# Optimization experiments

Measured on AMD Instinct MI355X. Metric: run time of the kernel, lower is better.

## Reference

```python
import jax, jax.numpy as jnp
import numpy as np

N_NODES = 100000
N_EDGES = 1600000
N_GRAPHS = 256
DIMS = [128, 128, 128, 128]  # gcn_layers_dim -> 3 GCNConv layers


def setup_inputs() -> dict:
    key = jax.random.key(0)
    ks = jax.random.split(key, 12)
    inp = {
        "x": jax.random.normal(ks[0], (N_NODES, DIMS[0]), jnp.float32),
        "edge_index": jax.random.randint(ks[1], (2, N_EDGES), 0, N_NODES),
        "edge_weight": jax.random.uniform(ks[2], (N_EDGES,), jnp.float32),
        "batch": jnp.sort(jax.random.randint(ks[3], (N_NODES,), 0, N_GRAPHS)),
    }
    for i in range(3):
        fan_in = DIMS[i]
        scale = 1.0 / np.sqrt(fan_in)
        inp[f"W{i+1}"] = jax.random.uniform(ks[4 + 2 * i], (DIMS[i], DIMS[i + 1]),
                                             jnp.float32, -scale, scale)
        inp[f"b{i+1}"] = jax.random.uniform(ks[5 + 2 * i], (DIMS[i + 1],),
                                             jnp.float32, -scale, scale)
    return inp


def reference(x, edge_index, edge_weight, batch, W1, b1, W2, b2, W3, b3):
    n = x.shape[0]
    # PyG GCNConv: add self-loops with weight 1, symmetric normalization.
    loop = jnp.arange(n)
    row = jnp.concatenate([edge_index[0], loop])  # source nodes
    col = jnp.concatenate([edge_index[1], loop])  # target nodes (aggregation index)
    w = jnp.concatenate([edge_weight, jnp.ones((n,), x.dtype)])
    deg = jax.ops.segment_sum(w, col, num_segments=n)
    dinv = jnp.where(deg > 0, jax.lax.rsqrt(deg), jnp.zeros_like(deg))
    norm = dinv[row] * w * dinv[col]  # [E+N]

    # global_mean_pool setup
    counts = jax.ops.segment_sum(jnp.ones((n,), x.dtype), batch,
                                 num_segments=N_GRAPHS)
    counts = jnp.maximum(counts, 1.0)[:, None]

    def gcn_conv(h, W, b):
        hl = h @ W                      # linear projection first (PyG order)
        msg = hl[row] * norm[:, None]   # gather + edge scaling
        out = jax.ops.segment_sum(msg, col, num_segments=n)  # scatter-add
        return out + b

    embeddings = []
    h = x
    for W, b in ((W1, b1), (W2, b2), (W3, b3)):
        h = gcn_conv(h, W, b)
        h = jax.nn.relu(h)              # relu_layers_index = [0,1,2]
        emb = jax.ops.segment_sum(h, batch, num_segments=N_GRAPHS) / counts
        embeddings.append(emb)          # gep = global_mean_pool
    return tuple(embeddings)
```

## Files before the change

kernel.cpp:

```cpp
#include <hip/hip_runtime.h>


typedef short short8 __attribute__((ext_vector_type(8)));
typedef float f32x4  __attribute__((ext_vector_type(4)));

__device__ inline unsigned pack_bf16x2(float a, float b) {
    unsigned ua = __float_as_uint(a);
    ua = (ua + 0x7FFFu + ((ua >> 16) & 1u)) >> 16;
    unsigned ub = __float_as_uint(b);
    ub = (ub + 0x7FFFu + ((ub >> 16) & 1u)) >> 16;
    return ua | (ub << 16);
}
__device__ inline ushort bf16_1(float a) {
    unsigned ua = __float_as_uint(a);
    return (ushort)((ua + 0x7FFFu + ((ua >> 16) & 1u)) >> 16);
}
__device__ inline float bf_lo(unsigned u) { return __uint_as_float(u << 16); }
__device__ inline float bf_hi(unsigned u) { return __uint_as_float(u & 0xFFFF0000u); }

__global__ void k_zero(int* __restrict__ cnt, int N) {
    int i = blockIdx.x * blockDim.x + threadIdx.x;
    if (i < N) cnt[i] = 0;
}

__global__ void k_phase1(const int* __restrict__ ei, int* __restrict__ cnt,
                         int* __restrict__ epos, int E) {
    int e = blockIdx.x * blockDim.x + threadIdx.x;
    if (e >= E) return;
    int c = ei[E + e];
    epos[e] = atomicAdd(&cnt[c], 1);
}

__global__ __launch_bounds__(1024) void k_scan1(const int* __restrict__ cnt,
                                                int* __restrict__ pre,
                                                int* __restrict__ bsum, int n) {
    __shared__ int wsum[16];
    int t = threadIdx.x, lane = t & 63, w = t >> 6;
    int i = blockIdx.x * 1024 + t;
    int v = (i < n) ? cnt[i] : 0;
    int x = v;
#pragma unroll
    for (int off = 1; off < 64; off <<= 1) {
        int y = __shfl_up(x, off, 64);
        if (lane >= off) x += y;
    }
    if (lane == 63) wsum[w] = x;
    __syncthreads();
    int woff = 0, tot = 0;
#pragma unroll
    for (int q = 0; q < 16; q++) { int s = wsum[q]; if (q < w) woff += s; tot += s; }
    if (i < n) pre[i] = woff + x - v;
    if (t == 0) bsum[blockIdx.x] = tot;
}

__global__ __launch_bounds__(128) void k_scan2(int* __restrict__ bsum, int nb,
                                               int* __restrict__ ptrv, int n) {
    __shared__ int ws[2];
    int t = threadIdx.x, lane = t & 63, w = t >> 6;
    int v = (t < nb) ? bsum[t] : 0;
    int x = v;
#pragma unroll
    for (int off = 1; off < 64; off <<= 1) {
        int y = __shfl_up(x, off, 64);
        if (lane >= off) x += y;
    }
    if (lane == 63) ws[w] = x;
    __syncthreads();
    int woff = (w == 1) ? ws[0] : 0;
    int tot = ws[0] + ws[1];
    if (t < nb) bsum[t] = woff + x - v;
    if (t == 0) ptrv[n] = tot;
}

__global__ __launch_bounds__(1024) void k_scan3(const int* __restrict__ pre,
                                                const int* __restrict__ bsum,
                                                int* __restrict__ ptrv, int n) {
    int i = blockIdx.x * 1024 + threadIdx.x;
    if (i >= n) return;
    ptrv[i] = pre[i] + bsum[blockIdx.x];
}

__global__ void k_scatter(const int* __restrict__ ei, const float* __restrict__ ew,
                          const int* __restrict__ ptrv, const int* __restrict__ epos,
                          int2* __restrict__ csr, int E) {
    int e = blockIdx.x * blockDim.x + threadIdx.x;
    if (e >= E) return;
    int r = ei[e];
    int c = ei[E + e];
    int2 v; v.x = r; v.y = __float_as_int(ew[e]);
    csr[ptrv[c] + epos[e]] = v;
}

__global__ void k_degdinv(const int2* __restrict__ csr, const int* __restrict__ ptrv,
                          float* __restrict__ dinv, int N) {
    int i = blockIdx.x * blockDim.x + threadIdx.x;
    if (i >= N) return;
    float s = 1.0f;
    int e1 = ptrv[i + 1];
    for (int j = ptrv[i]; j < e1; j++) s += __int_as_float(csr[j].y);
    dinv[i] = (s > 0.f) ? rsqrtf(s) : 0.f;
}

__global__ void k_norm(int2* __restrict__ csr, const int* __restrict__ ptrv,
                       const float* __restrict__ dinv, int N) {
    int i = blockIdx.x * blockDim.x + threadIdx.x;
    if (i >= N) return;
    float dc = dinv[i];
    int e1 = ptrv[i + 1];
    for (int j = ptrv[i]; j < e1; j++) {
        int2 m = csr[j];
        m.y = __float_as_int(dinv[m.x] * __int_as_float(m.y) * dc);
        csr[j] = m;
    }
}

__global__ void k_bounds(const int* __restrict__ batch, int* __restrict__ gb,
                         int N, int G) {
    int t = blockIdx.x * blockDim.x + threadIdx.x;
    if (t > G) return;
    int lo = 0, hi = N;
    while (lo < hi) { int mid = (lo + hi) >> 1; if (batch[mid] < t) lo = mid + 1; else hi = mid; }
    gb[t] = lo;
}

__global__ void k_wprep(const float* __restrict__ W0, const float* __restrict__ W1,
                        const float* __restrict__ W2, ushort* __restrict__ WbT) {
    int l = blockIdx.y;
    const float* W = (l == 0) ? W0 : ((l == 1) ? W1 : W2);
    int id = blockIdx.x * 256 + threadIdx.x;
    int n = id & 127, k = id >> 7;
    WbT[l * 16384 + n * 128 + k] = bf16_1(W[k * 128 + n]);
}

template <bool F32IN>
__global__ __launch_bounds__(256) void k_gemm_mfma(const void* __restrict__ Hin,
                                                   const ushort* __restrict__ WbT,
                                                   unsigned* __restrict__ O, int M) {
    __shared__ unsigned sOut[4 * 32 * 64];
    int lane = threadIdx.x & 63;
    int wv = threadIdx.x >> 6;
    int quad = lane >> 4;
    int mrow = lane & 15;
    int m0 = blockIdx.x * 128 + wv * 32;
    int r0 = m0 + mrow;
    int r1 = r0 + 16;
    int r0c = r0 < M ? r0 : M - 1;
    int r1c = r1 < M ? r1 : M - 1;

    short8 a0[4], a1[4];
    if (F32IN) {
        const float* Hf = (const float*)Hin;
#pragma unroll
        for (int s = 0; s < 4; s++) {
            const float4* p0 = (const float4*)(Hf + (size_t)r0c * 128 + s * 32 + quad * 8);
            const float4* p1 = (const float4*)(Hf + (size_t)r1c * 128 + s * 32 + quad * 8);
            float4 f0 = p0[0], f1 = p0[1];
            float4 g0 = p1[0], g1 = p1[1];
            union { short8 s8; unsigned u[4]; } t0, t1;
            t0.u[0] = pack_bf16x2(f0.x, f0.y); t0.u[1] = pack_bf16x2(f0.z, f0.w);
            t0.u[2] = pack_bf16x2(f1.x, f1.y); t0.u[3] = pack_bf16x2(f1.z, f1.w);
            t1.u[0] = pack_bf16x2(g0.x, g0.y); t1.u[1] = pack_bf16x2(g0.z, g0.w);
            t1.u[2] = pack_bf16x2(g1.x, g1.y); t1.u[3] = pack_bf16x2(g1.z, g1.w);
            a0[s] = t0.s8; a1[s] = t1.s8;
        }
    } else {
        const unsigned* Hb = (const unsigned*)Hin;
#pragma unroll
        for (int s = 0; s < 4; s++) {
            a0[s] = *(const short8*)(Hb + (size_t)r0c * 64 + s * 16 + quad * 4);
            a1[s] = *(const short8*)(Hb + (size_t)r1c * 64 + s * 16 + quad * 4);
        }
    }
    f32x4 acc0[8], acc1[8];
#pragma unroll
    for (int t = 0; t < 8; t++) {
        acc0[t] = (f32x4){0.f, 0.f, 0.f, 0.f};
        acc1[t] = (f32x4){0.f, 0.f, 0.f, 0.f};
    }
#pragma unroll
    for (int s = 0; s < 4; s++) {
#pragma unroll
        for (int t = 0; t < 8; t++) {
            short8 b = *(const short8*)(WbT + (t * 16 + mrow) * 128 + s * 32 + quad * 8);
            acc0[t] = __builtin_amdgcn_mfma_f32_16x16x32_bf16(a0[s], b, acc0[t], 0, 0, 0);
            acc1[t] = __builtin_amdgcn_mfma_f32_16x16x32_bf16(a1[s], b, acc1[t], 0, 0, 0);
        }
    }
    ushort* so = (ushort*)(sOut + wv * 32 * 64);
#pragma unroll
    for (int t = 0; t < 8; t++) {
#pragma unroll
        for (int r = 0; r < 4; r++) {
            int lr = quad * 4 + r;
            int c = t * 16 + mrow;
            so[lr * 128 + c] = bf16_1(acc0[t][r]);
            so[(lr + 16) * 128 + c] = bf16_1(acc1[t][r]);
        }
    }
    __syncthreads();
    const unsigned* si = sOut + wv * 32 * 64;
#pragma unroll 8
    for (int r = 0; r < 32; r++) {
        int row = m0 + r;
        if (row < M) O[(size_t)row * 64 + lane] = si[r * 64 + lane];
    }
}

__global__ __launch_bounds__(256) void k_agg(const unsigned* __restrict__ HL,
                                             const int* __restrict__ ptr,
                                             const int2* __restrict__ csr,
                                             const float* __restrict__ dinv,
                                             const float* __restrict__ bias,
                                             unsigned* __restrict__ Hout, int M) {
    __shared__ int2 sM[4 * 64];
    int node = (int)((blockIdx.x * blockDim.x + threadIdx.x) >> 6);
    if (node >= M) return;
    int lane = threadIdx.x & 63;
    int half = lane >> 5;
    int q = lane & 31;
    int2* mbase = &sM[(threadIdx.x >> 6) * 64];
    int e0 = ptr[node], e1 = ptr[node + 1];
    int deg = e1 - e0;
    int nbv = deg < 64 ? deg : 64;
    if (lane < nbv) mbase[lane] = csr[e0 + lane];
    const uint2* HL2 = (const uint2*)HL;
    float di = dinv[node];
    float sn = (half == 0) ? di * di : 0.f;
    uint2 us = HL2[(size_t)node * 32 + q];
    float a0 = sn * bf_lo(us.x), a1 = sn * bf_hi(us.x);
    float a2 = sn * bf_lo(us.y), a3 = sn * bf_hi(us.y);
    int j = half;
    for (; j + 8 <= nbv; j += 8) {
        int2 m[4]; uint2 u[4];
#pragma unroll
        for (int t = 0; t < 4; t++) m[t] = mbase[j + 2 * t];
#pragma unroll
        for (int t = 0; t < 4; t++) u[t] = HL2[(size_t)m[t].x * 32 + q];
#pragma unroll
        for (int t = 0; t < 4; t++) {
            float nv = __int_as_float(m[t].y);
            a0 += nv * bf_lo(u[t].x); a1 += nv * bf_hi(u[t].x);
            a2 += nv * bf_lo(u[t].y); a3 += nv * bf_hi(u[t].y);
        }
    }
    for (; j < nbv; j += 2) {
        int2 m = mbase[j];
        uint2 u = HL2[(size_t)m.x * 32 + q];
        float nv = __int_as_float(m.y);
        a0 += nv * bf_lo(u.x); a1 += nv * bf_hi(u.x);
        a2 += nv * bf_lo(u.y); a3 += nv * bf_hi(u.y);
    }
    for (int e = e0 + 64 + half; e < e1; e += 2) {
        int2 m = csr[e];
        uint2 u = HL2[(size_t)m.x * 32 + q];
        float nv = __int_as_float(m.y);
        a0 += nv * bf_lo(u.x); a1 += nv * bf_hi(u.x);
        a2 += nv * bf_lo(u.y); a3 += nv * bf_hi(u.y);
    }
    a0 += __shfl_xor(a0, 32, 64);
    a1 += __shfl_xor(a1, 32, 64);
    a2 += __shfl_xor(a2, 32, 64);
    a3 += __shfl_xor(a3, 32, 64);
    float4 bv = ((const float4*)bias)[q];
    float r0 = fmaxf(a0 + bv.x, 0.f);
    float r1 = fmaxf(a1 + bv.y, 0.f);
    float r2 = fmaxf(a2 + bv.z, 0.f);
    float r3 = fmaxf(a3 + bv.w, 0.f);
    if (half == 0) {
        uint2 pv;
        pv.x = pack_bf16x2(r0, r1);
        pv.y = pack_bf16x2(r2, r3);
        ((uint2*)(Hout + (size_t)node * 64))[q] = pv;
    }
}

__global__ __launch_bounds__(256) void k_pool(const unsigned* __restrict__ HB,
                                              const int* __restrict__ gb,
                                              float* __restrict__ outp) {
    __shared__ float part[4][128];
    int g = blockIdx.x;
    int lane = threadIdx.x & 63, w = threadIdx.x >> 6;
    int s = gb[g], e = gb[g + 1];
    float ax = 0.f, ay = 0.f;
    for (int i = s + w; i < e; i += 4) {
        unsigned u = HB[(size_t)i * 64 + lane];
        ax += bf_lo(u); ay += bf_hi(u);
    }
    part[w][lane * 2] = ax;
    part[w][lane * 2 + 1] = ay;
    __syncthreads();
    if (threadIdx.x < 128) {
        float sum = part[0][threadIdx.x] + part[1][threadIdx.x]
                  + part[2][threadIdx.x] + part[3][threadIdx.x];
        float c = (float)(e - s);
        outp[g * 128 + threadIdx.x] = sum / fmaxf(c, 1.0f);
    }
}

extern "C" void kernel_launch(void* const* d_in, const int* in_sizes, int n_in,
                              void* d_out, int out_size, void* d_ws, size_t ws_size,
                              hipStream_t stream) {
    const float* x     = (const float*)d_in[0];
    const int*   ei    = (const int*)d_in[1];
    const float* ew    = (const float*)d_in[2];
    const int*   batch = (const int*)d_in[3];
    const float* Wt[3] = {(const float*)d_in[4], (const float*)d_in[6], (const float*)d_in[8]};
    const float* bt[3] = {(const float*)d_in[5], (const float*)d_in[7], (const float*)d_in[9]};
    float* out = (float*)d_out;

    const int D = 128;
    const int N = in_sizes[0] / D;
    const int E = in_sizes[2];
    const int G = out_size / (3 * D);

    char* p = (char*)d_ws;
    auto alloc = [&](size_t bytes) {
        void* r = (void*)p;
        p += (bytes + 255) & ~(size_t)255;
        return r;
    };
    int*      cnt    = (int*)alloc((size_t)N * 4);
    int*      ptr    = (int*)alloc((size_t)(N + 1) * 4);
    int*      pre    = (int*)alloc((size_t)N * 4);
    int*      bsum   = (int*)alloc((size_t)128 * 4);
    int*      gb     = (int*)alloc((size_t)(G + 1) * 4);
    float*    dinv   = (float*)alloc((size_t)N * 4);
    ushort*   WbT    = (ushort*)alloc((size_t)3 * 16384 * 2);
    int2*     csr    = (int2*)alloc((size_t)E * 8);
    unsigned* bufHL  = (unsigned*)alloc((size_t)N * 64 * 4);
    unsigned* bufH   = (unsigned*)alloc((size_t)N * 64 * 4);
    int*      epos   = (int*)bufH;

    int nb = (N + 1023) / 1024;

    k_zero<<<(N + 255) / 256, 256, 0, stream>>>(cnt, N);
    k_phase1<<<(E + 255) / 256, 256, 0, stream>>>(ei, cnt, epos, E);
    k_bounds<<<1, 512, 0, stream>>>(batch, gb, N, G);
    k_wprep<<<dim3(64, 3), 256, 0, stream>>>(Wt[0], Wt[1], Wt[2], WbT);
    k_scan1<<<nb, 1024, 0, stream>>>(cnt, pre, bsum, N);
    k_scan2<<<1, 128, 0, stream>>>(bsum, nb, ptr, N);
    k_scan3<<<nb, 1024, 0, stream>>>(pre, bsum, ptr, N);
    k_scatter<<<(E + 255) / 256, 256, 0, stream>>>(ei, ew, ptr, epos, csr, E);
    k_degdinv<<<(N + 255) / 256, 256, 0, stream>>>(csr, ptr, dinv, N);
    k_norm<<<(N + 255) / 256, 256, 0, stream>>>(csr, ptr, dinv, N);

    for (int l = 0; l < 3; l++) {
        if (l == 0)
            k_gemm_mfma<true><<<(N + 127) / 128, 256, 0, stream>>>(x, WbT, bufHL, N);
        else
            k_gemm_mfma<false><<<(N + 127) / 128, 256, 0, stream>>>(bufH, WbT + (size_t)l * 16384,
                                                                    bufHL, N);
        k_agg<<<(N + 3) / 4, 256, 0, stream>>>(bufHL, ptr, csr, dinv, bt[l], bufH, N);
        k_pool<<<G, 256, 0, stream>>>(bufH, gb, out + (size_t)l * G * D);
    }
}
```

Before: 600.7 us.

## Merge prep kernels, fold x bf16 cast into phase1, warp-parallel deg/norm

Combines the zero, bounds and weight-prep kernels into one launch. The fp32-to-bf16 cast of x moves into the edge-counting kernel so the first GEMM reads bf16 like the later layers. The degree and normalization kernels switch from one thread per node to 32 lanes per node with a shuffle reduction, which spreads the edge loop and coalesces CSR reads. This removes launches and serial per-thread loops, but it adds an extra bf16 copy of x in memory and a full write/read pass over it. It also drops the deg>0 guard, relying on the self-loop keeping s at least 1.

Measured after the change: 597.0 us. No clear change (-0.6%).

```diff
diff --git a/kernel.cpp b/kernel.cpp
--- a/kernel.cpp
+++ b/kernel.cpp
@@ -18,17 +18,43 @@
 __device__ inline float bf_lo(unsigned u) { return __uint_as_float(u << 16); }
 __device__ inline float bf_hi(unsigned u) { return __uint_as_float(u & 0xFFFF0000u); }
 
-__global__ void k_zero(int* __restrict__ cnt, int N) {
-    int i = blockIdx.x * blockDim.x + threadIdx.x;
-    if (i < N) cnt[i] = 0;
+__global__ void k_prep(int* __restrict__ cnt, int N,
+                       const int* __restrict__ batch, int* __restrict__ gb, int G,
+                       const float* __restrict__ W0, const float* __restrict__ W1,
+                       const float* __restrict__ W2, ushort* __restrict__ WbT) {
+    int id = blockIdx.x * blockDim.x + threadIdx.x;
+    if (id < N) cnt[id] = 0;
+    if (id <= G) {
+        int lo = 0, hi = N;
+        while (lo < hi) { int mid = (lo + hi) >> 1; if (batch[mid] < id) lo = mid + 1; else hi = mid; }
+        gb[id] = lo;
+    }
+    if (id < 3 * 16384) {
+        int l = id >> 14;
+        const float* W = (l == 0) ? W0 : ((l == 1) ? W1 : W2);
+        int id2 = id & 16383;
+        int n = id2 & 127, k = id2 >> 7;
+        WbT[l * 16384 + n * 128 + k] = bf16_1(W[k * 128 + n]);
+    }
 }
 
 __global__ void k_phase1(const int* __restrict__ ei, int* __restrict__ cnt,
-                         int* __restrict__ epos, int E) {
-    int e = blockIdx.x * blockDim.x + threadIdx.x;
-    if (e >= E) return;
-    int c = ei[E + e];
-    epos[e] = atomicAdd(&cnt[c], 1);
+                         int* __restrict__ epos, int E,
+                         const float4* __restrict__ x4, uint2* __restrict__ xb2,
+                         int nCast) {
+    int tid = blockIdx.x * blockDim.x + threadIdx.x;
+    if (tid < E) {
+        int c = ei[E + tid];
+        epos[tid] = atomicAdd(&cnt[c], 1);
+    }
+    int stride = gridDim.x * blockDim.x;
+    for (int i = tid; i < nCast; i += stride) {
+        float4 f = x4[i];
+        uint2 v;
+        v.x = pack_bf16x2(f.x, f.y);
+        v.y = pack_bf16x2(f.z, f.w);
+        xb2[i] = v;
+    }
 }
 
 __global__ __launch_bounds__(1024) void k_scan1(const int* __restrict__ cnt,
@@ -91,49 +117,36 @@
     csr[ptrv[c] + epos[e]] = v;
 }
 
-__global__ void k_degdinv(const int2* __restrict__ csr, const int* __restrict__ ptrv,
-                          float* __restrict__ dinv, int N) {
-    int i = blockIdx.x * blockDim.x + threadIdx.x;
-    if (i >= N) return;
-    float s = 1.0f;
-    int e1 = ptrv[i + 1];
-    for (int j = ptrv[i]; j < e1; j++) s += __int_as_float(csr[j].y);
-    dinv[i] = (s > 0.f) ? rsqrtf(s) : 0.f;
-}
-
-__global__ void k_norm(int2* __restrict__ csr, const int* __restrict__ ptrv,
-                       const float* __restrict__ dinv, int N) {
-    int i = blockIdx.x * blockDim.x + threadIdx.x;
-    if (i >= N) return;
-    float dc = dinv[i];
-    int e1 = ptrv[i + 1];
-    for (int j = ptrv[i]; j < e1; j++) {
-        int2 m = csr[j];
+__global__ __launch_bounds__(256) void k_degdinv(const int2* __restrict__ csr,
+                                                 const int* __restrict__ ptrv,
+                                                 float* __restrict__ dinv, int N) {
+    int node = blockIdx.x * 8 + (threadIdx.x >> 5);
+    int j = threadIdx.x & 31;
+    if (node >= N) return;
+    int e0 = ptrv[node], e1 = ptrv[node + 1];
+    float s = (j == 0) ? 1.0f : 0.0f;
+    for (int e = e0 + j; e < e1; e += 32) s += __int_as_float(csr[e].y);
+#pragma unroll
+    for (int off = 1; off < 32; off <<= 1) s += __shfl_xor(s, off, 64);
+    if (j == 0) dinv[node] = rsqrtf(s);
+}
+
+__global__ __launch_bounds__(256) void k_norm(int2* __restrict__ csr,
+                                              const int* __restrict__ ptrv,
+                                              const float* __restrict__ dinv, int N) {
+    int node = blockIdx.x * 8 + (threadIdx.x >> 5);
+    int j = threadIdx.x & 31;
+    if (node >= N) return;
+    float dc = dinv[node];
+    int e0 = ptrv[node], e1 = ptrv[node + 1];
+    for (int e = e0 + j; e < e1; e += 32) {
+        int2 m = csr[e];
         m.y = __float_as_int(dinv[m.x] * __int_as_float(m.y) * dc);
-        csr[j] = m;
-    }
-}
-
-__global__ void k_bounds(const int* __restrict__ batch, int* __restrict__ gb,
-                         int N, int G) {
-    int t = blockIdx.x * blockDim.x + threadIdx.x;
-    if (t > G) return;
-    int lo = 0, hi = N;
-    while (lo < hi) { int mid = (lo + hi) >> 1; if (batch[mid] < t) lo = mid + 1; else hi = mid; }
-    gb[t] = lo;
-}
-
-__global__ void k_wprep(const float* __restrict__ W0, const float* __restrict__ W1,
-                        const float* __restrict__ W2, ushort* __restrict__ WbT) {
-    int l = blockIdx.y;
-    const float* W = (l == 0) ? W0 : ((l == 1) ? W1 : W2);
-    int id = blockIdx.x * 256 + threadIdx.x;
-    int n = id & 127, k = id >> 7;
-    WbT[l * 16384 + n * 128 + k] = bf16_1(W[k * 128 + n]);
-}
-
-template <bool F32IN>
-__global__ __launch_bounds__(256) void k_gemm_mfma(const void* __restrict__ Hin,
+        csr[e] = m;
+    }
+}
+
+__global__ __launch_bounds__(256) void k_gemm_mfma(const unsigned* __restrict__ Hb,
                                                    const ushort* __restrict__ WbT,
                                                    unsigned* __restrict__ O, int M) {
     __shared__ unsigned sOut[4 * 32 * 64];
@@ -148,28 +161,10 @@
     int r1c = r1 < M ? r1 : M - 1;
 
     short8 a0[4], a1[4];
-    if (F32IN) {
-        const float* Hf = (const float*)Hin;
-#pragma unroll
-        for (int s = 0; s < 4; s++) {
-            const float4* p0 = (const float4*)(Hf + (size_t)r0c * 128 + s * 32 + quad * 8);
-            const float4* p1 = (const float4*)(Hf + (size_t)r1c * 128 + s * 32 + quad * 8);
-            float4 f0 = p0[0], f1 = p0[1];
-            float4 g0 = p1[0], g1 = p1[1];
-            union { short8 s8; unsigned u[4]; } t0, t1;
-            t0.u[0] = pack_bf16x2(f0.x, f0.y); t0.u[1] = pack_bf16x2(f0.z, f0.w);
-            t0.u[2] = pack_bf16x2(f1.x, f1.y); t0.u[3] = pack_bf16x2(f1.z, f1.w);
-            t1.u[0] = pack_bf16x2(g0.x, g0.y); t1.u[1] = pack_bf16x2(g0.z, g0.w);
-            t1.u[2] = pack_bf16x2(g1.x, g1.y); t1.u[3] = pack_bf16x2(g1.z, g1.w);
-            a0[s] = t0.s8; a1[s] = t1.s8;
-        }
-    } else {
-        const unsigned* Hb = (const unsigned*)Hin;
-#pragma unroll
-        for (int s = 0; s < 4; s++) {
-            a0[s] = *(const short8*)(Hb + (size_t)r0c * 64 + s * 16 + quad * 4);
-            a1[s] = *(const short8*)(Hb + (size_t)r1c * 64 + s * 16 + quad * 4);
-        }
+#pragma unroll
+    for (int s = 0; s < 4; s++) {
+        a0[s] = *(const short8*)(Hb + (size_t)r0c * 64 + s * 16 + quad * 4);
+        a1[s] = *(const short8*)(Hb + (size_t)r1c * 64 + s * 16 + quad * 4);
     }
     f32x4 acc0[8], acc1[8];
 #pragma unroll
@@ -327,29 +322,29 @@
     float*    dinv   = (float*)alloc((size_t)N * 4);
     ushort*   WbT    = (ushort*)alloc((size_t)3 * 16384 * 2);
     int2*     csr    = (int2*)alloc((size_t)E * 8);
+    unsigned* xb     = (unsigned*)alloc((size_t)N * 64 * 4);
     unsigned* bufHL  = (unsigned*)alloc((size_t)N * 64 * 4);
     unsigned* bufH   = (unsigned*)alloc((size_t)N * 64 * 4);
     int*      epos   = (int*)bufH;
 
     int nb = (N + 1023) / 1024;
-
-    k_zero<<<(N + 255) / 256, 256, 0, stream>>>(cnt, N);
-    k_phase1<<<(E + 255) / 256, 256, 0, stream>>>(ei, cnt, epos, E);
-    k_bounds<<<1, 512, 0, stream>>>(batch, gb, N, G);
-    k_wprep<<<dim3(64, 3), 256, 0, stream>>>(Wt[0], Wt[1], Wt[2], WbT);
+    int prepWork = N > 3 * 16384 ? N : 3 * 16384;
+
+    k_prep<<<(prepWork + 255) / 256, 256, 0, stream>>>(cnt, N, batch, gb, G,
+                                                       Wt[0], Wt[1], Wt[2], WbT);
+    k_phase1<<<(E + 255) / 256, 256, 0, stream>>>(ei, cnt, epos, E,
+                                                  (const float4*)x, (uint2*)xb, N * 32);
     k_scan1<<<nb, 1024, 0, stream>>>(cnt, pre, bsum, N);
     k_scan2<<<1, 128, 0, stream>>>(bsum, nb, ptr, N);
     k_scan3<<<nb, 1024, 0, stream>>>(pre, bsum, ptr, N);
     k_scatter<<<(E + 255) / 256, 256, 0, stream>>>(ei, ew, ptr, epos, csr, E);
-    k_degdinv<<<(N + 255) / 256, 256, 0, stream>>>(csr, ptr, dinv, N);
-    k_norm<<<(N + 255) / 256, 256, 0, stream>>>(csr, ptr, dinv, N);
+    k_degdinv<<<(N + 7) / 8, 256, 0, stream>>>(csr, ptr, dinv, N);
+    k_norm<<<(N + 7) / 8, 256, 0, stream>>>(csr, ptr, dinv, N);
 
     for (int l = 0; l < 3; l++) {
-        if (l == 0)
-            k_gemm_mfma<true><<<(N + 127) / 128, 256, 0, stream>>>(x, WbT, bufHL, N);
-        else
-            k_gemm_mfma<false><<<(N + 127) / 128, 256, 0, stream>>>(bufH, WbT + (size_t)l * 16384,
-                                                                    bufHL, N);
+        const unsigned* hin = (l == 0) ? xb : bufH;
+        k_gemm_mfma<<<(N + 127) / 128, 256, 0, stream>>>(hin, WbT + (size_t)l * 16384,
+                                                         bufHL, N);
         k_agg<<<(N + 3) / 4, 256, 0, stream>>>(bufHL, ptr, csr, dinv, bt[l], bufH, N);
         k_pool<<<G, 256, 0, stream>>>(bufH, gb, out + (size_t)l * G * D);
     }
```
